# Kernel tuning notes

Measured on AMD Instinct MI355X. Metric: run time of the kernel, lower is better.

The kernel has to match this reference:

```python
import jax, jax.numpy as jnp
import numpy as np

B, S, HID = 1, 2048, 2048
NH, NKV, D = 32, 8, 64
GROUPS = NH // NKV
THETA = 10000.0


def _rope_tables(seq_len, dim):
    inv_freq = 1.0 / (THETA ** (jnp.arange(0, dim, 2, dtype=jnp.float32) / dim))
    t = jnp.arange(seq_len, dtype=jnp.float32)
    freqs = jnp.outer(t, inv_freq)            # [S, D/2]
    emb = jnp.concatenate([freqs, freqs], axis=-1)  # [S, D]
    return jnp.cos(emb), jnp.sin(emb)


def _rotate_half(x):
    x1, x2 = jnp.split(x, 2, axis=-1)
    return jnp.concatenate([-x2, x1], axis=-1)


def setup_inputs() -> dict:
    key = jax.random.key(0)
    ks = jax.random.split(key, 8)
    hidden_states = jax.random.normal(ks[0], (B, S, HID), dtype=jnp.float32)
    # additive causal mask, 0 on/below diagonal, -1e9 above
    causal = jnp.tril(jnp.ones((S, S), dtype=bool))
    attention_mask = jnp.where(causal, 0.0, -1e9).astype(jnp.float32)[None, None]
    sc = 0.02
    Wq = sc * jax.random.normal(ks[1], (NH * D, HID), dtype=jnp.float32)
    bq = jnp.zeros((NH * D,), dtype=jnp.float32)
    Wk = sc * jax.random.normal(ks[2], (NKV * D, HID), dtype=jnp.float32)
    bk = jnp.zeros((NKV * D,), dtype=jnp.float32)
    Wv = sc * jax.random.normal(ks[3], (NKV * D, HID), dtype=jnp.float32)
    bv = jnp.zeros((NKV * D,), dtype=jnp.float32)
    Wo = sc * jax.random.normal(ks[4], (HID, NH * D), dtype=jnp.float32)
    return {"hidden_states": hidden_states, "attention_mask": attention_mask,
            "Wq": Wq, "bq": bq, "Wk": Wk, "bk": bk, "Wv": Wv, "bv": bv, "Wo": Wo}


def reference(hidden_states, attention_mask, Wq, bq, Wk, bk, Wv, bv, Wo):
    b, s, _ = hidden_states.shape
    q = (hidden_states @ Wq.T + bq).reshape(b, s, NH, D).transpose(0, 2, 1, 3)   # [B,NH,S,D]
    k = (hidden_states @ Wk.T + bk).reshape(b, s, NKV, D).transpose(0, 2, 1, 3)  # [B,NKV,S,D]
    v = (hidden_states @ Wv.T + bv).reshape(b, s, NKV, D).transpose(0, 2, 1, 3)
    cos, sin = _rope_tables(s, D)
    cos = cos[None, None]; sin = sin[None, None]
    q = q * cos + _rotate_half(q) * sin
    k = k * cos + _rotate_half(k) * sin
    # GQA: repeat KV heads to match query heads
    k = jnp.repeat(k, GROUPS, axis=1)  # [B,NH,S,D]
    v = jnp.repeat(v, GROUPS, axis=1)
    scores = jnp.einsum('bhqd,bhkd->bhqk', q, k) / jnp.sqrt(jnp.float32(D))
    scores = jnp.clip(scores, -50.0, 50.0)
    scores = scores + attention_mask
    probs = jax.nn.softmax(scores.astype(jnp.float32), axis=-1).astype(q.dtype)
    attn = jnp.einsum('bhqk,bhkd->bhqd', probs, v)
    attn = attn.transpose(0, 2, 1, 3).reshape(b, s, NH * D)
    return attn @ Wo.T
```

## Files before the change

### kernel.cpp

```cpp
#include <hip/hip_runtime.h>
#include <hip/hip_bf16.h>
#include <stdint.h>

typedef unsigned short u16;
typedef unsigned int u32;

#define S_LEN 2048
#define HID 2048
#define NH 32
#define NKV 8
#define HD 64
#define PIT 2080

using f32x4 = __attribute__((ext_vector_type(4))) float;
using bfrag = __attribute__((ext_vector_type(8))) short;

__device__ __forceinline__ float b2f(u16 u) {
  union { u32 i; float f; } c; c.i = ((u32)u) << 16; return c.f;
}
__device__ __forceinline__ u16 f2b(float f) {
  union { float f; u32 i; } c; c.f = f;
  u32 r = c.i + 0x7fffu + ((c.i >> 16) & 1u);
  return (u16)(r >> 16);
}
__device__ __forceinline__ uint4 cvt8(const float* __restrict__ p) {
  float4 a = *(const float4*)p;
  float4 b = *(const float4*)(p + 4);
  uint4 r;
  r.x = (u32)f2b(a.x) | ((u32)f2b(a.y) << 16);
  r.y = (u32)f2b(a.z) | ((u32)f2b(a.w) << 16);
  r.z = (u32)f2b(b.x) | ((u32)f2b(b.y) << 16);
  r.w = (u32)f2b(b.z) | ((u32)f2b(b.w) << 16);
  return r;
}

__device__ __forceinline__ void gl2lds16(const u16* g, u16* l) {
  __builtin_amdgcn_global_load_lds(
      (const __attribute__((address_space(1))) void*)g,
      (__attribute__((address_space(3))) void*)l,
      16, 0, 0);
}

__global__ void conv_all(const float* __restrict__ hid, const float* __restrict__ Wq,
                         const float* __restrict__ Wk, const float* __restrict__ Wv,
                         u16* __restrict__ hidb, u16* __restrict__ Wqkvb) {
  int row = blockIdx.x;
  int col = threadIdx.x * 8;
  const float* src; u16* dst;
  if (row < 2048)      { src = hid + (size_t)row * 2048;          dst = hidb  + (size_t)row * PIT; }
  else if (row < 4096) { src = Wq + (size_t)(row - 2048) * 2048;  dst = Wqkvb + (size_t)(row - 2048) * PIT; }
  else if (row < 4608) { src = Wk + (size_t)(row - 4096) * 2048;  dst = Wqkvb + (size_t)(row - 4096 + 2048) * PIT; }
  else                 { src = Wv + (size_t)(row - 4608) * 2048;  dst = Wqkvb + (size_t)(row - 4608 + 2560) * PIT; }
  *(uint4*)(dst + col) = cvt8(src + col);
}

__global__ void conv_f2b_p(const float* __restrict__ in, u16* __restrict__ out, int n8) {
  int i = blockIdx.x * 256 + threadIdx.x;
  if (i >= n8) return;
  int row = i >> 8;
  int col = (i & 255) * 8;
  *(uint4*)(out + (size_t)row * PIT + col) = cvt8(in + (size_t)row * 2048 + col);
}

__global__ __launch_bounds__(256, 3) void gemm_qkv(
    const u16* __restrict__ A, const u16* __restrict__ B,
    const float* __restrict__ bq, const float* __restrict__ bk, const float* __restrict__ bv,
    u16* __restrict__ Qb, u16* __restrict__ Kb, u16* __restrict__ Vt)
{
  __shared__ __align__(16) u16 As[2 * 2048];
  __shared__ __align__(16) u16 Bs[2 * 4096];
  __shared__ __align__(16) u16 strip_s[4][16 * 72];

  const int tid  = threadIdx.x;
  const int m0   = blockIdx.y * 64;
  const int n0   = blockIdx.x * 128;
  const int lane = tid & 63;
  const int w    = tid >> 6;
  const int wm   = w >> 1, wn = w & 1;
  const int quad = lane >> 4, l16 = lane & 15;

  const int srow = tid >> 2;
  const int scol = (tid & 3) * 8;
  const u16* ga = A + (size_t)(m0 + srow) * PIT + scol;
  const u16* gb = B + (size_t)(n0 + srow) * PIT + scol;

  f32x4 zero = {0.f, 0.f, 0.f, 0.f};
  f32x4 acc[2][4];
#pragma unroll
  for (int mi = 0; mi < 2; ++mi)
#pragma unroll
    for (int ni = 0; ni < 4; ++ni) acc[mi][ni] = zero;

  gl2lds16(ga, As + tid * 8);
  gl2lds16(gb, Bs + tid * 8);
  gl2lds16(gb + (size_t)64 * PIT, Bs + 2048 + tid * 8);
  __syncthreads();

  int cur = 0;
  for (int k0 = 0; k0 < HID; k0 += 32) {
    if (k0 + 32 < HID) {
      u16* la = As + (cur ^ 1) * 2048 + tid * 8;
      u16* lb = Bs + (cur ^ 1) * 4096 + tid * 8;
      gl2lds16(ga + k0 + 32, la);
      gl2lds16(gb + k0 + 32, lb);
      gl2lds16(gb + (size_t)64 * PIT + k0 + 32, lb + 2048);
    }
    const u16* as = As + cur * 2048;
    const u16* bs = Bs + cur * 4096;

    bfrag af[2], bf[4];
#pragma unroll
    for (int i = 0; i < 2; ++i)
      af[i] = *(const bfrag*)&as[(wm * 32 + i * 16 + l16) * 32 + quad * 8];
#pragma unroll
    for (int i = 0; i < 4; ++i)
      bf[i] = *(const bfrag*)&bs[(wn * 64 + i * 16 + l16) * 32 + quad * 8];
#pragma unroll
    for (int mi = 0; mi < 2; ++mi)
#pragma unroll
      for (int ni = 0; ni < 4; ++ni)
        acc[mi][ni] = __builtin_amdgcn_mfma_f32_16x16x32_bf16(af[mi], bf[ni], acc[mi][ni], 0, 0, 0);

    __syncthreads();
    cur ^= 1;
  }

  u16* strip = strip_s[w];
  const int rr = lane >> 2;
  const int co = (lane & 3) * 8;

  if (n0 < 2048) {
#pragma unroll
    for (int mi = 0; mi < 2; ++mi) {
#pragma unroll
      for (int n01 = 0; n01 < 2; ++n01)
#pragma unroll
        for (int i = 0; i < 4; ++i) {
          int d  = n01 * 16 + l16;
          int c1 = n0 + wn * 64 + d;
          float x1 = acc[mi][n01][i]     + bq[c1];
          float x2 = acc[mi][n01 + 2][i] + bq[c1 + 32];
          float inv = exp2f(-(float)d * 0.41524101186092034f);
          float ang = (float)(m0 + wm * 32 + mi * 16 + quad * 4 + i) * inv;
          float cs = cosf(ang), sn = sinf(ang);
          strip[(quad * 4 + i) * 72 + d]      = f2b(x1 * cs - x2 * sn);
          strip[(quad * 4 + i) * 72 + d + 32] = f2b(x2 * cs + x1 * sn);
        }
      uint4 v0 = *(const uint4*)&strip[rr * 72 + co];
      uint4 v1 = *(const uint4*)&strip[rr * 72 + 32 + co];
      size_t gb2 = (size_t)(m0 + wm * 32 + mi * 16 + rr) * 2048 + n0 + wn * 64;
      *(uint4*)(Qb + gb2 + co)      = v0;
      *(uint4*)(Qb + gb2 + 32 + co) = v1;
    }
  } else if (n0 < 2560) {
    int cb = (n0 - 2048) + wn * 64;
#pragma unroll
    for (int mi = 0; mi < 2; ++mi) {
#pragma unroll
      for (int n01 = 0; n01 < 2; ++n01)
#pragma unroll
        for (int i = 0; i < 4; ++i) {
          int d  = n01 * 16 + l16;
          int cg = cb + d;
          float x1 = acc[mi][n01][i]     + bk[cg];
          float x2 = acc[mi][n01 + 2][i] + bk[cg + 32];
          float inv = exp2f(-(float)d * 0.41524101186092034f);
          float ang = (float)(m0 + wm * 32 + mi * 16 + quad * 4 + i) * inv;
          float cs = cosf(ang), sn = sinf(ang);
          strip[(quad * 4 + i) * 72 + d]      = f2b(x1 * cs - x2 * sn);
          strip[(quad * 4 + i) * 72 + d + 32] = f2b(x2 * cs + x1 * sn);
        }
      uint4 v0 = *(const uint4*)&strip[rr * 72 + co];
      uint4 v1 = *(const uint4*)&strip[rr * 72 + 32 + co];
      size_t gb2 = (size_t)(m0 + wm * 32 + mi * 16 + rr) * 512 + cb;
      *(uint4*)(Kb + gb2 + co)      = v0;
      *(uint4*)(Kb + gb2 + 32 + co) = v1;
    }
  } else {
    int cgb = (n0 - 2560) + wn * 64;
#pragma unroll
    for (int ni = 0; ni < 4; ++ni) {
      float bvv = bv[cgb + ni * 16 + l16];
#pragma unroll
      for (int mi = 0; mi < 2; ++mi)
#pragma unroll
        for (int i = 0; i < 4; ++i)
          strip[l16 * 72 + mi * 16 + quad * 4 + i] = f2b(acc[mi][ni][i] + bvv);
      uint4 v0 = *(const uint4*)&strip[rr * 72 + co];
      size_t gb2 = (size_t)(cgb + ni * 16 + rr) * PIT + m0 + wm * 32;
      *(uint4*)(Vt + gb2 + co) = v0;
    }
  }
}

__global__ __launch_bounds__(256, 3) void gemm_o(
    const u16* __restrict__ A, const u16* __restrict__ B, float* __restrict__ C)
{
  __shared__ __align__(16) u16 As[2 * 2048];
  __shared__ __align__(16) u16 Bs[2 * 4096];

  const int tid  = threadIdx.x;
  const int m0   = blockIdx.y * 64;
  const int n0   = blockIdx.x * 128;
  const int lane = tid & 63;
  const int w    = tid >> 6;
  const int wm   = w >> 1, wn = w & 1;
  const int quad = lane >> 4, l16 = lane & 15;

  const int srow = tid >> 2;
  const int scol = (tid & 3) * 8;
  const u16* ga = A + (size_t)(m0 + srow) * PIT + scol;
  const u16* gb = B + (size_t)(n0 + srow) * PIT + scol;

  f32x4 zero = {0.f, 0.f, 0.f, 0.f};
  f32x4 acc[2][4];
#pragma unroll
  for (int mi = 0; mi < 2; ++mi)
#pragma unroll
    for (int ni = 0; ni < 4; ++ni) acc[mi][ni] = zero;

  gl2lds16(ga, As + tid * 8);
  gl2lds16(gb, Bs + tid * 8);
  gl2lds16(gb + (size_t)64 * PIT, Bs + 2048 + tid * 8);
  __syncthreads();

  int cur = 0;
  for (int k0 = 0; k0 < HID; k0 += 32) {
    if (k0 + 32 < HID) {
      u16* la = As + (cur ^ 1) * 2048 + tid * 8;
      u16* lb = Bs + (cur ^ 1) * 4096 + tid * 8;
      gl2lds16(ga + k0 + 32, la);
      gl2lds16(gb + k0 + 32, lb);
      gl2lds16(gb + (size_t)64 * PIT + k0 + 32, lb + 2048);
    }
    const u16* as = As + cur * 2048;
    const u16* bs = Bs + cur * 4096;

    bfrag af[2], bf[4];
#pragma unroll
    for (int i = 0; i < 2; ++i)
      af[i] = *(const bfrag*)&as[(wm * 32 + i * 16 + l16) * 32 + quad * 8];
#pragma unroll
    for (int i = 0; i < 4; ++i)
      bf[i] = *(const bfrag*)&bs[(wn * 64 + i * 16 + l16) * 32 + quad * 8];
#pragma unroll
    for (int mi = 0; mi < 2; ++mi)
#pragma unroll
      for (int ni = 0; ni < 4; ++ni)
        acc[mi][ni] = __builtin_amdgcn_mfma_f32_16x16x32_bf16(af[mi], bf[ni], acc[mi][ni], 0, 0, 0);

    __syncthreads();
    cur ^= 1;
  }

#pragma unroll
  for (int ni = 0; ni < 4; ++ni) {
    int col = n0 + wn * 64 + ni * 16 + l16;
#pragma unroll
    for (int mi = 0; mi < 2; ++mi)
#pragma unroll
      for (int i = 0; i < 4; ++i) {
        int row = m0 + wm * 32 + mi * 16 + quad * 4 + i;
        C[(size_t)row * 2048 + col] = acc[mi][ni][i];
      }
  }
}

#define SM_SC 0.18033688011112042f
#define SM_UB 72.134752044448169f

__global__ __launch_bounds__(256, 2) void attn_flash4(
    const u16* __restrict__ Qb, const u16* __restrict__ Kb,
    const u16* __restrict__ Vt, u16* __restrict__ Ab)
{
  __shared__ __align__(16) u16 Ks[2][64 * 64];
  __shared__ __align__(16) u16 Vs[2][64 * 64];
  __shared__ __align__(16) u16 Ps[4][2][16][72];

  const int h    = blockIdx.x;
  const int qbb  = 15 - (int)blockIdx.y;
  const int kvh  = h >> 2;
  const int tid  = threadIdx.x;
  const int lane = tid & 63;
  const int w    = tid >> 6;
  const int quad = lane >> 4, l16 = lane & 15;

  bfrag qf[2][2];
#pragma unroll
  for (int g = 0; g < 2; ++g) {
    const u16* qp = Qb + (size_t)(qbb * 128 + g * 64 + w * 16 + l16) * 2048 + h * 64 + quad * 8;
    qf[g][0] = *(const bfrag*)qp;
    qf[g][1] = *(const bfrag*)(qp + 32);
  }

  const int c0  = w * 128 + lane;
  const int r0  = c0 >> 3,        s0 = c0 & 7;
  const int r1  = (c0 + 64) >> 3, s1 = (c0 + 64) & 7;
  const int sg0 = s0 ^ (r0 & 7);
  const int sg1 = s1 ^ (r1 & 7);
  const u16* Ksrc0 = Kb + (size_t)r0 * 512 + kvh * 64 + sg0 * 8;
  const u16* Ksrc1 = Kb + (size_t)r1 * 512 + kvh * 64 + sg1 * 8;
  const u16* Vsrc0 = Vt + (size_t)(kvh * 64 + r0) * PIT + sg0 * 8;
  const u16* Vsrc1 = Vt + (size_t)(kvh * 64 + r1) * PIT + sg1 * 8;

#define STAGEKV(buf, kb)                                                        \
  do {                                                                          \
    gl2lds16(Ksrc0 + (size_t)(kb) * 32768, &Ks[buf][0] + c0 * 8);               \
    gl2lds16(Ksrc1 + (size_t)(kb) * 32768, &Ks[buf][0] + (c0 + 64) * 8);        \
    gl2lds16(Vsrc0 + (kb) * 64,            &Vs[buf][0] + c0 * 8);               \
    gl2lds16(Vsrc1 + (kb) * 64,            &Vs[buf][0] + (c0 + 64) * 8);        \
  } while (0)

  f32x4 zero = {0.f, 0.f, 0.f, 0.f};
  f32x4 o_acc[2][4];
  float lpart[2][4];
#pragma unroll
  for (int g = 0; g < 2; ++g)
#pragma unroll
    for (int nb = 0; nb < 4; ++nb) { o_acc[g][nb] = zero; lpart[g][nb] = 0.f; }

#define QKT_SM_FULL(g)                                                          \
  do {                                                                          \
    f32x4 s_acc[4];                                                             \
    _Pragma("unroll")                                                           \
    for (int nb = 0; nb < 4; ++nb) {                                            \
      s_acc[nb] = __builtin_amdgcn_mfma_f32_16x16x32_bf16(qf[g][0], kf0[nb], zero, 0, 0, 0); \
      s_acc[nb] = __builtin_amdgcn_mfma_f32_16x16x32_bf16(qf[g][1], kf1[nb], s_acc[nb], 0, 0, 0); \
    }                                                                           \
    _Pragma("unroll")                                                           \
    for (int nb = 0; nb < 4; ++nb)                                              \
      _Pragma("unroll")                                                         \
      for (int i = 0; i < 4; ++i) {                                             \
        float u = s_acc[nb][i] * SM_SC;                                         \
        u = fminf(SM_UB, fmaxf(-SM_UB, u));                                     \
        float p = __builtin_amdgcn_exp2f(u);                                    \
        lpart[g][i] += p;                                                       \
        Ps[w][g][quad * 4 + i][nb * 16 + l16] = f2b(p);                         \
      }                                                                         \
  } while (0)

#define QKT_SM_DIAG(g)                                                          \
  do {                                                                          \
    f32x4 s_acc[4];                                                             \
    _Pragma("unroll")                                                           \
    for (int nb = 0; nb < 4; ++nb) {                                            \
      s_acc[nb] = __builtin_amdgcn_mfma_f32_16x16x32_bf16(qf[g][0], kf0[nb], zero, 0, 0, 0); \
      s_acc[nb] = __builtin_amdgcn_mfma_f32_16x16x32_bf16(qf[g][1], kf1[nb], s_acc[nb], 0, 0, 0); \
    }                                                                           \
    _Pragma("unroll")                                                           \
    for (int nb = 0; nb < 4; ++nb)                                              \
      _Pragma("unroll")                                                         \
      for (int i = 0; i < 4; ++i) {                                             \
        float u = s_acc[nb][i] * SM_SC;                                         \
        u = fminf(SM_UB, fmaxf(-SM_UB, u));                                     \
        bool msk = (nb * 16 + l16 > w * 16 + quad * 4 + i);                     \
        float p = msk ? 0.0f : __builtin_amdgcn_exp2f(u);                       \
        lpart[g][i] += p;                                                       \
        Ps[w][g][quad * 4 + i][nb * 16 + l16] = f2b(p);                         \
      }                                                                         \
  } while (0)

#define PVACC(g)                                                                \
  do {                                                                          \
    bfrag pf0 = *(const bfrag*)&Ps[w][g][l16][quad * 8];                        \
    bfrag pf1 = *(const bfrag*)&Ps[w][g][l16][32 + quad * 8];                   \
    _Pragma("unroll")                                                           \
    for (int nb = 0; nb < 4; ++nb) {                                            \
      o_acc[g][nb] = __builtin_amdgcn_mfma_f32_16x16x32_bf16(pf0, vf0[nb], o_acc[g][nb], 0, 0, 0); \
      o_acc[g][nb] = __builtin_amdgcn_mfma_f32_16x16x32_bf16(pf1, vf1[nb], o_acc[g][nb], 0, 0, 0); \
    }                                                                           \
  } while (0)

  const int bulk  = 2 * qbb;
  const int kbmax = bulk + 1;
  const int swz   = (l16 & 7) * 8;

  STAGEKV(0, 0);
  __syncthreads();

  int cur = 0;
  for (int kb = 0; kb <= kbmax; ++kb) {
    if (kb < kbmax) STAGEKV(cur ^ 1, kb + 1);

    const u16* ks = &Ks[cur][0];
    const u16* vs = &Vs[cur][0];

    bfrag kf0[4], kf1[4];
#pragma unroll
    for (int nb = 0; nb < 4; ++nb) {
      int row = (nb * 16 + l16) * 64;
      kf0[nb] = *(const bfrag*)&ks[row + ((quad * 8) ^ swz)];
      kf1[nb] = *(const bfrag*)&ks[row + ((32 + quad * 8) ^ swz)];
    }

    if (kb < bulk)        { QKT_SM_FULL(0); QKT_SM_FULL(1); }
    else if (kb == bulk)  { QKT_SM_DIAG(0); QKT_SM_FULL(1); }
    else                  { QKT_SM_DIAG(1); }

    bfrag vf0[4], vf1[4];
#pragma unroll
    for (int nb = 0; nb < 4; ++nb) {
      int row = (nb * 16 + l16) * 64;
      vf0[nb] = *(const bfrag*)&vs[row + ((quad * 8) ^ swz)];
      vf1[nb] = *(const bfrag*)&vs[row + ((32 + quad * 8) ^ swz)];
    }

    if (kb <= bulk) PVACC(0);
    PVACC(1);

    __syncthreads();
    cur ^= 1;
  }

#pragma unroll
  for (int off = 1; off < 16; off <<= 1)
#pragma unroll
    for (int g = 0; g < 2; ++g)
#pragma unroll
      for (int i = 0; i < 4; ++i)
        lpart[g][i] += __shfl_xor(lpart[g][i], off, 64);

#pragma unroll
  for (int g = 0; g < 2; ++g)
#pragma unroll
    for (int i = 0; i < 4; ++i) {
      float inv = 1.0f / lpart[g][i];
      size_t rbase = (size_t)(qbb * 128 + g * 64 + w * 16 + quad * 4 + i) * PIT + h * 64;
#pragma unroll
      for (int nb = 0; nb < 4; ++nb)
        Ab[rbase + nb * 16 + l16] = f2b(o_acc[g][nb][i] * inv);
    }
}

extern "C" void kernel_launch(void* const* d_in, const int* in_sizes, int n_in,
                              void* d_out, int out_size, void* d_ws, size_t ws_size,
                              hipStream_t stream) {
  const float* hid = (const float*)d_in[0];
  const float* Wq = (const float*)d_in[2];
  const float* bq = (const float*)d_in[3];
  const float* Wk = (const float*)d_in[4];
  const float* bk = (const float*)d_in[5];
  const float* Wv = (const float*)d_in[6];
  const float* bv = (const float*)d_in[7];
  const float* Wo = (const float*)d_in[8];

  u16* hidb  = (u16*)d_ws;
  u16* Wqkvb = hidb + (size_t)2048 * PIT;
  u16* Qb    = Wqkvb + (size_t)3072 * PIT;
  u16* Kb    = Qb + 4194304;
  u16* Vt    = Kb + 1048576;
  u16* Wob   = hidb;
  u16* Ab    = Wqkvb;
  float* Ob  = (float*)d_out;

  conv_all<<<5120, 256, 0, stream>>>(hid, Wq, Wk, Wv, hidb, Wqkvb);

  gemm_qkv<<<dim3(24, 32), 256, 0, stream>>>(hidb, Wqkvb, bq, bk, bv, Qb, Kb, Vt);

  conv_f2b_p<<<2048, 256, 0, stream>>>(Wo, Wob, 524288);

  attn_flash4<<<dim3(32, 16), 256, 0, stream>>>(Qb, Kb, Vt, Ab);

  gemm_o<<<dim3(16, 32), 256, 0, stream>>>(Ab, Wob, Ob);
}
```

Before: 279.0 us.

## Use 2-wave 128-thread blocks with 64x64 per-wave tiles in projection GEMMs

Both projection GEMMs keep the same 64x128 block tile but now run it with 2 waves instead of 4. Each wave computes a 64x64 sub-tile (4x4 MFMA accumulators instead of 2x4), and each thread issues twice as many global-to-LDS loads per stage. The aim is more data reuse per wave (fewer LDS fragment reads per MFMA) and less barrier overhead. The cost is more accumulator registers, fewer waves per block for hiding latency, and a tighter occupancy bound.

```diff
diff --git a/kernel.cpp b/kernel.cpp
--- a/kernel.cpp
+++ b/kernel.cpp
@@ -62,61 +62,62 @@
   *(uint4*)(out + (size_t)row * PIT + col) = cvt8(in + (size_t)row * 2048 + col);
 }
 
-__global__ __launch_bounds__(256, 3) void gemm_qkv(
+__global__ __launch_bounds__(128, 2) void gemm_qkv(
     const u16* __restrict__ A, const u16* __restrict__ B,
     const float* __restrict__ bq, const float* __restrict__ bk, const float* __restrict__ bv,
     u16* __restrict__ Qb, u16* __restrict__ Kb, u16* __restrict__ Vt)
 {
   __shared__ __align__(16) u16 As[2 * 2048];
   __shared__ __align__(16) u16 Bs[2 * 4096];
-  __shared__ __align__(16) u16 strip_s[4][16 * 72];
+  __shared__ __align__(16) u16 strip_s[2][16 * 72];
 
   const int tid  = threadIdx.x;
   const int m0   = blockIdx.y * 64;
   const int n0   = blockIdx.x * 128;
   const int lane = tid & 63;
   const int w    = tid >> 6;
-  const int wm   = w >> 1, wn = w & 1;
   const int quad = lane >> 4, l16 = lane & 15;
 
-  const int srow = tid >> 2;
-  const int scol = (tid & 3) * 8;
-  const u16* ga = A + (size_t)(m0 + srow) * PIT + scol;
-  const u16* gb = B + (size_t)(n0 + srow) * PIT + scol;
+  const u16* gA = A + (size_t)(m0 + (tid >> 2)) * PIT + (tid & 3) * 8;
+  const u16* gB = B + (size_t)(n0 + (tid >> 2)) * PIT + (tid & 3) * 8;
+
+#define STAGE_QKV(buf, k0)                                                      \
+  do {                                                                          \
+    u16* la = As + (buf) * 2048 + tid * 8;                                      \
+    u16* lb = Bs + (buf) * 4096 + tid * 8;                                      \
+    gl2lds16(gA + (k0), la);                                                    \
+    gl2lds16(gA + (size_t)32 * PIT + (k0), la + 1024);                          \
+    gl2lds16(gB + (k0), lb);                                                    \
+    gl2lds16(gB + (size_t)32 * PIT + (k0), lb + 1024);                          \
+    gl2lds16(gB + (size_t)64 * PIT + (k0), lb + 2048);                          \
+    gl2lds16(gB + (size_t)96 * PIT + (k0), lb + 3072);                          \
+  } while (0)
 
   f32x4 zero = {0.f, 0.f, 0.f, 0.f};
-  f32x4 acc[2][4];
-#pragma unroll
-  for (int mi = 0; mi < 2; ++mi)
+  f32x4 acc[4][4];
+#pragma unroll
+  for (int mi = 0; mi < 4; ++mi)
 #pragma unroll
     for (int ni = 0; ni < 4; ++ni) acc[mi][ni] = zero;
 
-  gl2lds16(ga, As + tid * 8);
-  gl2lds16(gb, Bs + tid * 8);
-  gl2lds16(gb + (size_t)64 * PIT, Bs + 2048 + tid * 8);
+  STAGE_QKV(0, 0);
   __syncthreads();
 
   int cur = 0;
   for (int k0 = 0; k0 < HID; k0 += 32) {
-    if (k0 + 32 < HID) {
-      u16* la = As + (cur ^ 1) * 2048 + tid * 8;
-      u16* lb = Bs + (cur ^ 1) * 4096 + tid * 8;
-      gl2lds16(ga + k0 + 32, la);
-      gl2lds16(gb + k0 + 32, lb);
-      gl2lds16(gb + (size_t)64 * PIT + k0 + 32, lb + 2048);
-    }
+    if (k0 + 32 < HID) STAGE_QKV(cur ^ 1, k0 + 32);
     const u16* as = As + cur * 2048;
-    const u16* bs = Bs + cur * 4096;
-
-    bfrag af[2], bf[4];
-#pragma unroll
-    for (int i = 0; i < 2; ++i)
-      af[i] = *(const bfrag*)&as[(wm * 32 + i * 16 + l16) * 32 + quad * 8];
+    const u16* bs = Bs + cur * 4096 + w * 2048;
+
+    bfrag af[4], bf[4];
 #pragma unroll
     for (int i = 0; i < 4; ++i)
-      bf[i] = *(const bfrag*)&bs[(wn * 64 + i * 16 + l16) * 32 + quad * 8];
-#pragma unroll
-    for (int mi = 0; mi < 2; ++mi)
+      af[i] = *(const bfrag*)&as[(i * 16 + l16) * 32 + quad * 8];
+#pragma unroll
+    for (int i = 0; i < 4; ++i)
+      bf[i] = *(const bfrag*)&bs[(i * 16 + l16) * 32 + quad * 8];
+#pragma unroll
+    for (int mi = 0; mi < 4; ++mi)
 #pragma unroll
       for (int ni = 0; ni < 4; ++ni)
         acc[mi][ni] = __builtin_amdgcn_mfma_f32_16x16x32_bf16(af[mi], bf[ni], acc[mi][ni], 0, 0, 0);
@@ -124,38 +125,40 @@
     __syncthreads();
     cur ^= 1;
   }
+#undef STAGE_QKV
 
   u16* strip = strip_s[w];
   const int rr = lane >> 2;
   const int co = (lane & 3) * 8;
 
   if (n0 < 2048) {
-#pragma unroll
-    for (int mi = 0; mi < 2; ++mi) {
+    int cb = n0 + w * 64;
+#pragma unroll
+    for (int mi = 0; mi < 4; ++mi) {
 #pragma unroll
       for (int n01 = 0; n01 < 2; ++n01)
 #pragma unroll
         for (int i = 0; i < 4; ++i) {
           int d  = n01 * 16 + l16;
-          int c1 = n0 + wn * 64 + d;
+          int c1 = cb + d;
           float x1 = acc[mi][n01][i]     + bq[c1];
           float x2 = acc[mi][n01 + 2][i] + bq[c1 + 32];
           float inv = exp2f(-(float)d * 0.41524101186092034f);
-          float ang = (float)(m0 + wm * 32 + mi * 16 + quad * 4 + i) * inv;
+          float ang = (float)(m0 + mi * 16 + quad * 4 + i) * inv;
           float cs = cosf(ang), sn = sinf(ang);
           strip[(quad * 4 + i) * 72 + d]      = f2b(x1 * cs - x2 * sn);
           strip[(quad * 4 + i) * 72 + d + 32] = f2b(x2 * cs + x1 * sn);
         }
       uint4 v0 = *(const uint4*)&strip[rr * 72 + co];
       uint4 v1 = *(const uint4*)&strip[rr * 72 + 32 + co];
-      size_t gb2 = (size_t)(m0 + wm * 32 + mi * 16 + rr) * 2048 + n0 + wn * 64;
+      size_t gb2 = (size_t)(m0 + mi * 16 + rr) * 2048 + cb;
       *(uint4*)(Qb + gb2 + co)      = v0;
       *(uint4*)(Qb + gb2 + 32 + co) = v1;
     }
   } else if (n0 < 2560) {
-    int cb = (n0 - 2048) + wn * 64;
-#pragma unroll
-    for (int mi = 0; mi < 2; ++mi) {
+    int cb = (n0 - 2048) + w * 64;
+#pragma unroll
+    for (int mi = 0; mi < 4; ++mi) {
 #pragma unroll
       for (int n01 = 0; n01 < 2; ++n01)
 #pragma unroll
@@ -165,35 +168,37 @@
           float x1 = acc[mi][n01][i]     + bk[cg];
           float x2 = acc[mi][n01 + 2][i] + bk[cg + 32];
           float inv = exp2f(-(float)d * 0.41524101186092034f);
-          float ang = (float)(m0 + wm * 32 + mi * 16 + quad * 4 + i) * inv;
+          float ang = (float)(m0 + mi * 16 + quad * 4 + i) * inv;
           float cs = cosf(ang), sn = sinf(ang);
           strip[(quad * 4 + i) * 72 + d]      = f2b(x1 * cs - x2 * sn);
           strip[(quad * 4 + i) * 72 + d + 32] = f2b(x2 * cs + x1 * sn);
         }
       uint4 v0 = *(const uint4*)&strip[rr * 72 + co];
       uint4 v1 = *(const uint4*)&strip[rr * 72 + 32 + co];
-      size_t gb2 = (size_t)(m0 + wm * 32 + mi * 16 + rr) * 512 + cb;
+      size_t gb2 = (size_t)(m0 + mi * 16 + rr) * 512 + cb;
       *(uint4*)(Kb + gb2 + co)      = v0;
       *(uint4*)(Kb + gb2 + 32 + co) = v1;
     }
   } else {
-    int cgb = (n0 - 2560) + wn * 64;
+    int cgb = (n0 - 2560) + w * 64;
 #pragma unroll
     for (int ni = 0; ni < 4; ++ni) {
       float bvv = bv[cgb + ni * 16 + l16];
 #pragma unroll
-      for (int mi = 0; mi < 2; ++mi)
+      for (int mi = 0; mi < 4; ++mi)
 #pragma unroll
         for (int i = 0; i < 4; ++i)
           strip[l16 * 72 + mi * 16 + quad * 4 + i] = f2b(acc[mi][ni][i] + bvv);
       uint4 v0 = *(const uint4*)&strip[rr * 72 + co];
-      size_t gb2 = (size_t)(cgb + ni * 16 + rr) * PIT + m0 + wm * 32;
-      *(uint4*)(Vt + gb2 + co) = v0;
-    }
-  }
-}
-
-__global__ __launch_bounds__(256, 3) void gemm_o(
+      uint4 v1 = *(const uint4*)&strip[rr * 72 + 32 + co];
+      size_t gb2 = (size_t)(cgb + ni * 16 + rr) * PIT + m0;
+      *(uint4*)(Vt + gb2 + co)      = v0;
+      *(uint4*)(Vt + gb2 + 32 + co) = v1;
+    }
+  }
+}
+
+__global__ __launch_bounds__(128, 2) void gemm_o(
     const u16* __restrict__ A, const u16* __restrict__ B, float* __restrict__ C)
 {
   __shared__ __align__(16) u16 As[2 * 2048];
@@ -204,47 +209,48 @@
   const int n0   = blockIdx.x * 128;
   const int lane = tid & 63;
   const int w    = tid >> 6;
-  const int wm   = w >> 1, wn = w & 1;
   const int quad = lane >> 4, l16 = lane & 15;
 
-  const int srow = tid >> 2;
-  const int scol = (tid & 3) * 8;
-  const u16* ga = A + (size_t)(m0 + srow) * PIT + scol;
-  const u16* gb = B + (size_t)(n0 + srow) * PIT + scol;
+  const u16* gA = A + (size_t)(m0 + (tid >> 2)) * PIT + (tid & 3) * 8;
+  const u16* gB = B + (size_t)(n0 + (tid >> 2)) * PIT + (tid & 3) * 8;
+
+#define STAGE_O(buf, k0)                                                        \
+  do {                                                                          \
+    u16* la = As + (buf) * 2048 + tid * 8;                                      \
+    u16* lb = Bs + (buf) * 4096 + tid * 8;                                      \
+    gl2lds16(gA + (k0), la);                                                    \
+    gl2lds16(gA + (size_t)32 * PIT + (k0), la + 1024);                          \
+    gl2lds16(gB + (k0), lb);                                                    \
+    gl2lds16(gB + (size_t)32 * PIT + (k0), lb + 1024);                          \
+    gl2lds16(gB + (size_t)64 * PIT + (k0), lb + 2048);                          \
+    gl2lds16(gB + (size_t)96 * PIT + (k0), lb + 3072);                          \
+  } while (0)
 
   f32x4 zero = {0.f, 0.f, 0.f, 0.f};
-  f32x4 acc[2][4];
-#pragma unroll
-  for (int mi = 0; mi < 2; ++mi)
+  f32x4 acc[4][4];
+#pragma unroll
+  for (int mi = 0; mi < 4; ++mi)
 #pragma unroll
     for (int ni = 0; ni < 4; ++ni) acc[mi][ni] = zero;
 
-  gl2lds16(ga, As + tid * 8);
-  gl2lds16(gb, Bs + tid * 8);
-  gl2lds16(gb + (size_t)64 * PIT, Bs + 2048 + tid * 8);
+  STAGE_O(0, 0);
   __syncthreads();
 
   int cur = 0;
   for (int k0 = 0; k0 < HID; k0 += 32) {
-    if (k0 + 32 < HID) {
-      u16* la = As + (cur ^ 1) * 2048 + tid * 8;
-      u16* lb = Bs + (cur ^ 1) * 4096 + tid * 8;
-      gl2lds16(ga + k0 + 32, la);
-      gl2lds16(gb + k0 + 32, lb);
-      gl2lds16(gb + (size_t)64 * PIT + k0 + 32, lb + 2048);
-    }
+    if (k0 + 32 < HID) STAGE_O(cur ^ 1, k0 + 32);
     const u16* as = As + cur * 2048;
-    const u16* bs = Bs + cur * 4096;
-
-    bfrag af[2], bf[4];
-#pragma unroll
-    for (int i = 0; i < 2; ++i)
-      af[i] = *(const bfrag*)&as[(wm * 32 + i * 16 + l16) * 32 + quad * 8];
+    const u16* bs = Bs + cur * 4096 + w * 2048;
+
+    bfrag af[4], bf[4];
 #pragma unroll
     for (int i = 0; i < 4; ++i)
-      bf[i] = *(const bfrag*)&bs[(wn * 64 + i * 16 + l16) * 32 + quad * 8];
-#pragma unroll
-    for (int mi = 0; mi < 2; ++mi)
+      af[i] = *(const bfrag*)&as[(i * 16 + l16) * 32 + quad * 8];
+#pragma unroll
+    for (int i = 0; i < 4; ++i)
+      bf[i] = *(const bfrag*)&bs[(i * 16 + l16) * 32 + quad * 8];
+#pragma unroll
+    for (int mi = 0; mi < 4; ++mi)
 #pragma unroll
       for (int ni = 0; ni < 4; ++ni)
         acc[mi][ni] = __builtin_amdgcn_mfma_f32_16x16x32_bf16(af[mi], bf[ni], acc[mi][ni], 0, 0, 0);
@@ -252,15 +258,16 @@
     __syncthreads();
     cur ^= 1;
   }
+#undef STAGE_O
 
 #pragma unroll
   for (int ni = 0; ni < 4; ++ni) {
-    int col = n0 + wn * 64 + ni * 16 + l16;
-#pragma unroll
-    for (int mi = 0; mi < 2; ++mi)
+    int col = n0 + w * 64 + ni * 16 + l16;
+#pragma unroll
+    for (int mi = 0; mi < 4; ++mi)
 #pragma unroll
       for (int i = 0; i < 4; ++i) {
-        int row = m0 + wm * 32 + mi * 16 + quad * 4 + i;
+        int row = m0 + mi * 16 + quad * 4 + i;
         C[(size_t)row * 2048 + col] = acc[mi][ni][i];
       }
   }
@@ -455,11 +462,11 @@
 
   conv_all<<<5120, 256, 0, stream>>>(hid, Wq, Wk, Wv, hidb, Wqkvb);
 
-  gemm_qkv<<<dim3(24, 32), 256, 0, stream>>>(hidb, Wqkvb, bq, bk, bv, Qb, Kb, Vt);
+  gemm_qkv<<<dim3(24, 32), 128, 0, stream>>>(hidb, Wqkvb, bq, bk, bv, Qb, Kb, Vt);
 
   conv_f2b_p<<<2048, 256, 0, stream>>>(Wo, Wob, 524288);
 
   attn_flash4<<<dim3(32, 16), 256, 0, stream>>>(Qb, Kb, Vt, Ab);
 
-  gemm_o<<<dim3(16, 32), 256, 0, stream>>>(Ab, Wob, Ob);
-}
+  gemm_o<<<dim3(16, 32), 128, 0, stream>>>(Ab, Wob, Ob);
+}
```

Result: slower. 458.2 us (+64.2%).

## Triple-buffer LDS staging with vmcnt-based waits in GEMMs and attention

Applied to the files above, without the earlier changes.

The QKV GEMM, the output GEMM and the flash-attention kernel move from double to triple buffering of their LDS tiles. Loads are issued two stages ahead. Each loop iteration now uses one partial `s_waitcnt vmcnt(N)` plus a single barrier, replacing the previous full drain and end-of-loop `__syncthreads`. In attention, the Q register loads now come after the first two KV prefetches so those prefetches start earlier. The aim is to hide global-to-LDS latency behind MFMA work, at the cost of more LDS per block, which may pressure occupancy. Correctness now depends on hand-counted vmcnt values.

```diff
diff --git a/kernel.cpp b/kernel.cpp
--- a/kernel.cpp
+++ b/kernel.cpp
@@ -40,6 +40,8 @@
       (__attribute__((address_space(3))) void*)l,
       16, 0, 0);
 }
+
+#define WAITBAR(N) asm volatile("s_waitcnt vmcnt(" #N ")\ns_barrier" ::: "memory")
 
 __global__ void conv_all(const float* __restrict__ hid, const float* __restrict__ Wq,
                          const float* __restrict__ Wk, const float* __restrict__ Wv,
@@ -67,8 +69,8 @@
     const float* __restrict__ bq, const float* __restrict__ bk, const float* __restrict__ bv,
     u16* __restrict__ Qb, u16* __restrict__ Kb, u16* __restrict__ Vt)
 {
-  __shared__ __align__(16) u16 As[2 * 2048];
-  __shared__ __align__(16) u16 Bs[2 * 4096];
+  __shared__ __align__(16) u16 As[3 * 2048];
+  __shared__ __align__(16) u16 Bs[3 * 4096];
   __shared__ __align__(16) u16 strip_s[4][16 * 72];
 
   const int tid  = threadIdx.x;
@@ -84,6 +86,13 @@
   const u16* ga = A + (size_t)(m0 + srow) * PIT + scol;
   const u16* gb = B + (size_t)(n0 + srow) * PIT + scol;
 
+#define STAGE_G(bi, k0)                                                         \
+  do {                                                                          \
+    gl2lds16(ga + (k0), As + (bi) * 2048 + tid * 8);                            \
+    gl2lds16(gb + (k0), Bs + (bi) * 4096 + tid * 8);                            \
+    gl2lds16(gb + (size_t)64 * PIT + (k0), Bs + (bi) * 4096 + 2048 + tid * 8);  \
+  } while (0)
+
   f32x4 zero = {0.f, 0.f, 0.f, 0.f};
   f32x4 acc[2][4];
 #pragma unroll
@@ -91,19 +100,16 @@
 #pragma unroll
     for (int ni = 0; ni < 4; ++ni) acc[mi][ni] = zero;
 
-  gl2lds16(ga, As + tid * 8);
-  gl2lds16(gb, Bs + tid * 8);
-  gl2lds16(gb + (size_t)64 * PIT, Bs + 2048 + tid * 8);
-  __syncthreads();
+  STAGE_G(0, 0);
+  STAGE_G(1, 32);
 
   int cur = 0;
-  for (int k0 = 0; k0 < HID; k0 += 32) {
-    if (k0 + 32 < HID) {
-      u16* la = As + (cur ^ 1) * 2048 + tid * 8;
-      u16* lb = Bs + (cur ^ 1) * 4096 + tid * 8;
-      gl2lds16(ga + k0 + 32, la);
-      gl2lds16(gb + k0 + 32, lb);
-      gl2lds16(gb + (size_t)64 * PIT + k0 + 32, lb + 2048);
+  for (int k = 0; k < 64; ++k) {
+    if (k < 63) WAITBAR(3);
+    else        WAITBAR(0);
+    if (k + 2 < 64) {
+      int nb = cur + 2; if (nb >= 3) nb -= 3;
+      STAGE_G(nb, (k + 2) * 32);
     }
     const u16* as = As + cur * 2048;
     const u16* bs = Bs + cur * 4096;
@@ -121,9 +127,9 @@
       for (int ni = 0; ni < 4; ++ni)
         acc[mi][ni] = __builtin_amdgcn_mfma_f32_16x16x32_bf16(af[mi], bf[ni], acc[mi][ni], 0, 0, 0);
 
-    __syncthreads();
-    cur ^= 1;
-  }
+    cur += 1; if (cur == 3) cur = 0;
+  }
+#undef STAGE_G
 
   u16* strip = strip_s[w];
   const int rr = lane >> 2;
@@ -196,8 +202,8 @@
 __global__ __launch_bounds__(256, 3) void gemm_o(
     const u16* __restrict__ A, const u16* __restrict__ B, float* __restrict__ C)
 {
-  __shared__ __align__(16) u16 As[2 * 2048];
-  __shared__ __align__(16) u16 Bs[2 * 4096];
+  __shared__ __align__(16) u16 As[3 * 2048];
+  __shared__ __align__(16) u16 Bs[3 * 4096];
 
   const int tid  = threadIdx.x;
   const int m0   = blockIdx.y * 64;
@@ -212,6 +218,13 @@
   const u16* ga = A + (size_t)(m0 + srow) * PIT + scol;
   const u16* gb = B + (size_t)(n0 + srow) * PIT + scol;
 
+#define STAGE_G(bi, k0)                                                         \
+  do {                                                                          \
+    gl2lds16(ga + (k0), As + (bi) * 2048 + tid * 8);                            \
+    gl2lds16(gb + (k0), Bs + (bi) * 4096 + tid * 8);                            \
+    gl2lds16(gb + (size_t)64 * PIT + (k0), Bs + (bi) * 4096 + 2048 + tid * 8);  \
+  } while (0)
+
   f32x4 zero = {0.f, 0.f, 0.f, 0.f};
   f32x4 acc[2][4];
 #pragma unroll
@@ -219,19 +232,16 @@
 #pragma unroll
     for (int ni = 0; ni < 4; ++ni) acc[mi][ni] = zero;
 
-  gl2lds16(ga, As + tid * 8);
-  gl2lds16(gb, Bs + tid * 8);
-  gl2lds16(gb + (size_t)64 * PIT, Bs + 2048 + tid * 8);
-  __syncthreads();
+  STAGE_G(0, 0);
+  STAGE_G(1, 32);
 
   int cur = 0;
-  for (int k0 = 0; k0 < HID; k0 += 32) {
-    if (k0 + 32 < HID) {
-      u16* la = As + (cur ^ 1) * 2048 + tid * 8;
-      u16* lb = Bs + (cur ^ 1) * 4096 + tid * 8;
-      gl2lds16(ga + k0 + 32, la);
-      gl2lds16(gb + k0 + 32, lb);
-      gl2lds16(gb + (size_t)64 * PIT + k0 + 32, lb + 2048);
+  for (int k = 0; k < 64; ++k) {
+    if (k < 63) WAITBAR(3);
+    else        WAITBAR(0);
+    if (k + 2 < 64) {
+      int nb = cur + 2; if (nb >= 3) nb -= 3;
+      STAGE_G(nb, (k + 2) * 32);
     }
     const u16* as = As + cur * 2048;
     const u16* bs = Bs + cur * 4096;
@@ -249,9 +259,9 @@
       for (int ni = 0; ni < 4; ++ni)
         acc[mi][ni] = __builtin_amdgcn_mfma_f32_16x16x32_bf16(af[mi], bf[ni], acc[mi][ni], 0, 0, 0);
 
-    __syncthreads();
-    cur ^= 1;
-  }
+    cur += 1; if (cur == 3) cur = 0;
+  }
+#undef STAGE_G
 
 #pragma unroll
   for (int ni = 0; ni < 4; ++ni) {
@@ -269,12 +279,12 @@
 #define SM_SC 0.18033688011112042f
 #define SM_UB 72.134752044448169f
 
-__global__ __launch_bounds__(256, 2) void attn_flash4(
+__global__ __launch_bounds__(256, 2) void attn_flash5(
     const u16* __restrict__ Qb, const u16* __restrict__ Kb,
     const u16* __restrict__ Vt, u16* __restrict__ Ab)
 {
-  __shared__ __align__(16) u16 Ks[2][64 * 64];
-  __shared__ __align__(16) u16 Vs[2][64 * 64];
+  __shared__ __align__(16) u16 Ks[3][64 * 64];
+  __shared__ __align__(16) u16 Vs[3][64 * 64];
   __shared__ __align__(16) u16 Ps[4][2][16][72];
 
   const int h    = blockIdx.x;
@@ -284,14 +294,6 @@
   const int lane = tid & 63;
   const int w    = tid >> 6;
   const int quad = lane >> 4, l16 = lane & 15;
-
-  bfrag qf[2][2];
-#pragma unroll
-  for (int g = 0; g < 2; ++g) {
-    const u16* qp = Qb + (size_t)(qbb * 128 + g * 64 + w * 16 + l16) * 2048 + h * 64 + quad * 8;
-    qf[g][0] = *(const bfrag*)qp;
-    qf[g][1] = *(const bfrag*)(qp + 32);
-  }
 
   const int c0  = w * 128 + lane;
   const int r0  = c0 >> 3,        s0 = c0 & 7;
@@ -310,6 +312,20 @@
     gl2lds16(Vsrc0 + (kb) * 64,            &Vs[buf][0] + c0 * 8);               \
     gl2lds16(Vsrc1 + (kb) * 64,            &Vs[buf][0] + (c0 + 64) * 8);        \
   } while (0)
+
+  const int bulk  = 2 * qbb;
+  const int kbmax = bulk + 1;
+
+  STAGEKV(0, 0);
+  STAGEKV(1, 1);
+
+  bfrag qf[2][2];
+#pragma unroll
+  for (int g = 0; g < 2; ++g) {
+    const u16* qp = Qb + (size_t)(qbb * 128 + g * 64 + w * 16 + l16) * 2048 + h * 64 + quad * 8;
+    qf[g][0] = *(const bfrag*)qp;
+    qf[g][1] = *(const bfrag*)(qp + 32);
+  }
 
   f32x4 zero = {0.f, 0.f, 0.f, 0.f};
   f32x4 o_acc[2][4];
@@ -371,16 +387,16 @@
     }                                                                           \
   } while (0)
 
-  const int bulk  = 2 * qbb;
-  const int kbmax = bulk + 1;
-  const int swz   = (l16 & 7) * 8;
-
-  STAGEKV(0, 0);
-  __syncthreads();
+  const int swz = (l16 & 7) * 8;
 
   int cur = 0;
   for (int kb = 0; kb <= kbmax; ++kb) {
-    if (kb < kbmax) STAGEKV(cur ^ 1, kb + 1);
+    if (kb < kbmax) WAITBAR(4);
+    else            WAITBAR(0);
+    if (kb + 2 <= kbmax) {
+      int nb3 = cur + 2; if (nb3 >= 3) nb3 -= 3;
+      STAGEKV(nb3, kb + 2);
+    }
 
     const u16* ks = &Ks[cur][0];
     const u16* vs = &Vs[cur][0];
@@ -408,8 +424,7 @@
     if (kb <= bulk) PVACC(0);
     PVACC(1);
 
-    __syncthreads();
-    cur ^= 1;
+    cur += 1; if (cur == 3) cur = 0;
   }
 
 #pragma unroll
@@ -459,7 +474,7 @@
 
   conv_f2b_p<<<2048, 256, 0, stream>>>(Wo, Wob, 524288);
 
-  attn_flash4<<<dim3(32, 16), 256, 0, stream>>>(Qb, Kb, Vt, Ab);
+  attn_flash5<<<dim3(32, 16), 256, 0, stream>>>(Qb, Kb, Vt, Ab);
 
   gemm_o<<<dim3(16, 32), 256, 0, stream>>>(Ab, Wob, Ob);
 }
```

Result: faster. 262.3 us (-6.0%).
